# Kernel optimization log

Measured on AMD Instinct MI355X. Metric: run time of the kernel, lower is better.

Reference implementation:

```python
import jax, jax.numpy as jnp
import numpy as np

N0, N1, N2 = 331776, 36864, 4096   # src nodes block0, mid nodes, final items
E0, E1, EP = 294912, 32768, 4096   # edges block0, block1, pos/neg edges
F_RAW, D, H = 128, 256, 512        # raw feat dim, hidden_dims_sum, 2*hidden
N_NODES = 1000000                  # global graph node count (scorer bias)


def setup_inputs() -> dict:
    key = jax.random.key(0)
    ks = jax.random.split(key, 24)
    ri = lambda k, n, hi: jax.random.randint(k, (n,), 0, hi, dtype=jnp.int64 if False else jnp.int32).astype(jnp.int32)
    s = 0.05
    return {
        "feat0": jax.random.normal(ks[0], (N0, F_RAW), jnp.float32),
        "feat_dst": jax.random.normal(ks[1], (N2, F_RAW), jnp.float32),
        "weights0": jax.random.uniform(ks[2], (E0,), jnp.float32),
        "weights1": jax.random.uniform(ks[3], (E1,), jnp.float32),
        "W_proj": jax.random.normal(ks[4], (F_RAW, D), jnp.float32) * s,
        "b_proj": jnp.zeros((D,), jnp.float32),
        "Q1": jax.random.normal(ks[5], (D, H), jnp.float32) * s,
        "bq1": jnp.zeros((H,), jnp.float32),
        "W1": jax.random.normal(ks[6], (D + H, D), jnp.float32) * s,
        "bw1": jnp.zeros((D,), jnp.float32),
        "Q2": jax.random.normal(ks[7], (D, H), jnp.float32) * s,
        "bq2": jnp.zeros((H,), jnp.float32),
        "W2": jax.random.normal(ks[8], (D + H, D), jnp.float32) * s,
        "bw2": jnp.zeros((D,), jnp.float32),
        "bias": jnp.zeros((N_NODES,), jnp.float32),
        "block0_src": ri(ks[9], E0, N0),
        "block0_dst": ri(ks[10], E0, N1),
        "block1_src": ri(ks[11], E1, N1),
        "block1_dst": ri(ks[12], E1, N2),
        "pos_src": ri(ks[13], EP, N2),
        "pos_dst": ri(ks[14], EP, N2),
        "neg_src": ri(ks[15], EP, N2),
        "neg_dst": ri(ks[16], EP, N2),
        "nid": ri(ks[17], N2, N_NODES),
    }


def _l2norm(z):
    n = jnp.linalg.norm(z, axis=1, keepdims=True)
    return z / jnp.where(n == 0, 1.0, n)


def _sage_conv(h_src, h_dst, src, dst, w, Q, bq, W, bw, n_dst):
    # WeightedSAGEConv (dropout omitted: eval-mode deterministic reference)
    n = jax.nn.relu(h_src @ Q + bq)                                   # [N_src, H]
    m = jax.ops.segment_sum(n[src] * w[:, None], dst, num_segments=n_dst)
    ws = jnp.clip(jax.ops.segment_sum(w, dst, num_segments=n_dst), 1.0, None)
    z = jax.nn.relu(jnp.concatenate([m / ws[:, None], h_dst], axis=1) @ W + bw)
    return _l2norm(z)


def _score(h, src, dst, nid, bias):
    # ItemToItemScorer: u_dot_v + src/dst node bias
    return jnp.sum(h[src] * h[dst], axis=1) + bias[nid[src]] + bias[nid[dst]]


def reference(feat0, feat_dst, weights0, weights1, W_proj, b_proj, Q1, bq1, W1, bw1,
              Q2, bq2, W2, bw2, bias, block0_src, block0_dst, block1_src, block1_dst,
              pos_src, pos_dst, neg_src, neg_dst, nid):
    h = feat0 @ W_proj + b_proj                                         # LinearProjector
    h = _sage_conv(h, h[:N1], block0_src, block0_dst, weights0, Q1, bq1, W1, bw1, N1)
    h = _sage_conv(h, h[:N2], block1_src, block1_dst, weights1, Q2, bq2, W2, bw2, N2)
    h_item = (feat_dst @ W_proj + b_proj) + h                           # get_repr skip-add
    pos_score = _score(h_item, pos_src, pos_dst, nid, bias)
    neg_score = _score(h_item, neg_src, neg_dst, nid, bias)
    return (pos_score, neg_score)
```

## Files before the change

kernel.cpp:

```cpp
#include <hip/hip_runtime.h>
#include <hip/hip_bf16.h>

typedef __hip_bfloat16 bf16;
typedef __attribute__((ext_vector_type(8))) short frag8;
typedef __attribute__((ext_vector_type(4))) float f32x4;

#define N0c 331776
#define N1c 36864
#define N2c 4096
#define E0c 294912
#define E1c 32768

__device__ __forceinline__ float bfbits2f(unsigned short b) {
    union { unsigned u; float f; } x; x.u = ((unsigned)b) << 16; return x.f;
}
__device__ __forceinline__ unsigned short f2bfbits(float f) {
    bf16 h = __float2bfloat16(f);
    return *reinterpret_cast<unsigned short*>(&h);
}
__device__ __forceinline__ void load4f(const float* p, float* o) {
    const float4 v = *reinterpret_cast<const float4*>(p);
    o[0] = v.x; o[1] = v.y; o[2] = v.z; o[3] = v.w;
}
__device__ __forceinline__ ushort4 pack4(float4 v) {
    ushort4 o; o.x = f2bfbits(v.x); o.y = f2bfbits(v.y);
    o.z = f2bfbits(v.z); o.w = f2bfbits(v.w); return o;
}
__device__ __forceinline__ void store_c(float* p, float v) { *p = v; }
__device__ __forceinline__ void store_c(bf16* p, float v)  { *p = __float2bfloat16(v); }
__device__ __forceinline__ f32x4 zero4() {
    f32x4 z; z[0] = 0.f; z[1] = 0.f; z[2] = 0.f; z[3] = 0.f; return z;
}
__device__ __forceinline__ f32x4 mfma16(frag8 a, frag8 b, f32x4 c) {
    return __builtin_amdgcn_mfma_f32_16x16x32_bf16(a, b, c, 0, 0, 0);
}

__global__ __launch_bounds__(256) void transpose_bf16(
    const float* __restrict__ src, bf16* __restrict__ dst, int K, int N)
{
    const int idx = blockIdx.x * 256 + threadIdx.x;
    if (idx >= K * N) return;
    const int k = idx / N, n = idx - k * N;
    dst[(size_t)n * K + k] = __float2bfloat16(src[idx]);
}

__global__ __launch_bounds__(256) void hist_kernel(
    const int* __restrict__ dst, int* __restrict__ cnt, int E)
{
    const int e = blockIdx.x * 256 + threadIdx.x;
    if (e < E) atomicAdd(&cnt[dst[e]], 1);
}

__global__ __launch_bounds__(256) void scan_kernel(
    const int* __restrict__ cnt, int* __restrict__ base, int n)
{
    __shared__ int ps[256];
    const int t = threadIdx.x;
    const int chunk = (n + 255) >> 8;
    const int lo = t * chunk;
    const int hi = (lo + chunk < n) ? lo + chunk : n;
    int s = 0;
    for (int i = lo; i < hi; ++i) s += cnt[i];
    ps[t] = s;
    __syncthreads();
    for (int off = 1; off < 256; off <<= 1) {
        int v = (t >= off) ? ps[t - off] : 0;
        __syncthreads();
        ps[t] += v;
        __syncthreads();
    }
    int run = ps[t] - s;
    for (int i = lo; i < hi; ++i) { base[i] = run; run += cnt[i]; }
    if (t == 255) base[n] = ps[255];
}

__global__ __launch_bounds__(256) void fill_kernel(
    const int* __restrict__ dst, const int* __restrict__ base,
    int* __restrict__ cursor, int* __restrict__ perm, int E)
{
    const int e = blockIdx.x * 256 + threadIdx.x;
    if (e < E) {
        const int d = dst[e];
        const int p = base[d] + atomicAdd(&cursor[d], 1);
        perm[p] = e;
    }
}

template<typename TC>
__global__ __launch_bounds__(256) void gemm_mfma_proj(
    const float* __restrict__ A, const bf16* __restrict__ WpT,
    const float* __restrict__ bp, TC* __restrict__ C)
{
    __shared__ bf16 Xs[64 * 136];
    __shared__ bf16 Cs[64 * 264];

    const int tid = threadIdx.x;
    const int lane = tid & 63, wave = tid >> 6;
    const int row0 = blockIdx.x * 64;

    {
        const int r = tid >> 2, q = tid & 3;
        const float* ar = A + (size_t)(row0 + r) * 128 + q * 32;
        bf16* xr = Xs + r * 136 + q * 32;
        #pragma unroll
        for (int i = 0; i < 8; ++i)
            *reinterpret_cast<ushort4*>(xr + i * 4) =
                pack4(*reinterpret_cast<const float4*>(ar + i * 4));
    }
    __syncthreads();

    const int lr = lane & 15;
    const int lk = (lane >> 4) * 8;
    const int lm4 = (lane >> 4) * 4;

    f32x4 acc[4][4];
    #pragma unroll
    for (int mi = 0; mi < 4; ++mi)
        #pragma unroll
        for (int ni = 0; ni < 4; ++ni) acc[mi][ni] = zero4();

    #pragma unroll
    for (int kk = 0; kk < 4; ++kk) {
        frag8 a[4], b[4];
        #pragma unroll
        for (int mi = 0; mi < 4; ++mi)
            a[mi] = *reinterpret_cast<const frag8*>(&Xs[(mi * 16 + lr) * 136 + kk * 32 + lk]);
        #pragma unroll
        for (int ni = 0; ni < 4; ++ni)
            b[ni] = *reinterpret_cast<const frag8*>(
                WpT + (size_t)(wave * 64 + ni * 16 + lr) * 128 + kk * 32 + lk);
        #pragma unroll
        for (int mi = 0; mi < 4; ++mi)
            #pragma unroll
            for (int ni = 0; ni < 4; ++ni)
                acc[mi][ni] = mfma16(a[mi], b[ni], acc[mi][ni]);
    }

    if constexpr (sizeof(TC) == 2) {
        #pragma unroll
        for (int ni = 0; ni < 4; ++ni) {
            const int c = wave * 64 + ni * 16 + lr;
            const float bb = bp[c];
            #pragma unroll
            for (int mi = 0; mi < 4; ++mi)
                #pragma unroll
                for (int i = 0; i < 4; ++i)
                    Cs[(mi * 16 + lm4 + i) * 264 + c] =
                        __float2bfloat16(acc[mi][ni][i] + bb);
        }
        __syncthreads();
        const int r = tid >> 2, q = tid & 3;
        const bf16* sl = Cs + r * 264 + q * 64;
        bf16* dg = (bf16*)C + (size_t)(row0 + r) * 256 + q * 64;
        #pragma unroll
        for (int i = 0; i < 8; ++i)
            *reinterpret_cast<int4*>(dg + i * 8) =
                *reinterpret_cast<const int4*>(sl + i * 8);
    } else {
        #pragma unroll
        for (int ni = 0; ni < 4; ++ni) {
            const int c = wave * 64 + ni * 16 + lr;
            const float bb = bp[c];
            #pragma unroll
            for (int mi = 0; mi < 4; ++mi)
                #pragma unroll
                for (int i = 0; i < 4; ++i)
                    store_c(C + (size_t)(row0 + mi * 16 + lm4 + i) * 256 + c,
                            acc[mi][ni][i] + bb);
        }
    }
}

__global__ __launch_bounds__(256) void edge_csr(
    const bf16* __restrict__ zn, const bf16* __restrict__ QT,
    const float* __restrict__ bq,
    const int* __restrict__ perm, const int* __restrict__ src,
    const float* __restrict__ w,
    bf16* __restrict__ nbuf)
{
    __shared__ bf16 Zs[64 * 264];
    __shared__ bf16 Os[64 * 264];
    __shared__ int   srcs[64];
    __shared__ float wts[64];

    const int tid = threadIdx.x;
    const int lane = tid & 63, wave = tid >> 6;
    const size_t p0 = (size_t)blockIdx.x * 64;

    if (tid < 64) {
        const int e = perm[p0 + tid];
        srcs[tid] = src[e];
        wts[tid]  = w[e];
    }
    __syncthreads();

    {
        const int r = tid >> 2, q = tid & 3;
        const bf16* zr = zn + (size_t)srcs[r] * 256 + q * 64;
        bf16* zo = Zs + r * 264 + q * 64;
        #pragma unroll
        for (int i = 0; i < 16; ++i)
            *reinterpret_cast<ushort4*>(zo + i * 4) =
                *reinterpret_cast<const ushort4*>(zr + i * 4);
    }
    __syncthreads();

    const int lr = lane & 15;
    const int lk = (lane >> 4) * 8;
    const int lm4 = (lane >> 4) * 4;

    for (int pass = 0; pass < 2; ++pass) {
        const int nc0 = wave * 128 + pass * 64;
        f32x4 acc[4][4];
        #pragma unroll
        for (int mi = 0; mi < 4; ++mi)
            #pragma unroll
            for (int ni = 0; ni < 4; ++ni) acc[mi][ni] = zero4();

        #pragma unroll
        for (int kk = 0; kk < 8; ++kk) {
            frag8 a[4], b[4];
            #pragma unroll
            for (int mi = 0; mi < 4; ++mi)
                a[mi] = *reinterpret_cast<const frag8*>(&Zs[(mi * 16 + lr) * 264 + kk * 32 + lk]);
            #pragma unroll
            for (int ni = 0; ni < 4; ++ni)
                b[ni] = *reinterpret_cast<const frag8*>(
                    QT + (size_t)(nc0 + ni * 16 + lr) * 256 + kk * 32 + lk);
            #pragma unroll
            for (int mi = 0; mi < 4; ++mi)
                #pragma unroll
                for (int ni = 0; ni < 4; ++ni)
                    acc[mi][ni] = mfma16(a[mi], b[ni], acc[mi][ni]);
        }

        #pragma unroll
        for (int ni = 0; ni < 4; ++ni) {
            const int gc = nc0 + ni * 16 + lr;
            const float bb = bq[gc];
            const int lc = wave * 64 + ni * 16 + lr;
            #pragma unroll
            for (int mi = 0; mi < 4; ++mi)
                #pragma unroll
                for (int i = 0; i < 4; ++i) {
                    const int row = mi * 16 + lm4 + i;
                    const float val = fmaxf(acc[mi][ni][i] + bb, 0.f) * wts[row];
                    Os[row * 264 + lc] = __float2bfloat16(val);
                }
        }
        __syncthreads();

        {
            const int r = tid >> 2, q = tid & 3;
            const bf16* so = Os + r * 264 + q * 64;
            bf16* dg = nbuf + (p0 + r) * 512 + q * 128 + pass * 64;
            #pragma unroll
            for (int i = 0; i < 8; ++i)
                *reinterpret_cast<int4*>(dg + i * 8) =
                    *reinterpret_cast<const int4*>(so + i * 8);
        }
        __syncthreads();
    }
}

__global__ __launch_bounds__(256) void reduce_csr(
    const bf16* __restrict__ nbuf, const int* __restrict__ base,
    const int* __restrict__ perm, const float* __restrict__ w,
    bf16* __restrict__ mout)
{
    const int d = blockIdx.x;
    const int lo = base[d], hi = base[d + 1];
    __shared__ float s_inv;
    if (threadIdx.x == 0) {
        float s = 0.f;
        for (int k = lo; k < hi; ++k) s += w[perm[k]];
        s_inv = 1.f / fmaxf(s, 1.f);
    }
    __syncthreads();
    const int c = threadIdx.x * 2;
    float a0 = 0.f, a1 = 0.f;
    for (int k = lo; k < hi; ++k) {
        const ushort2 u = *reinterpret_cast<const ushort2*>(nbuf + (size_t)k * 512 + c);
        a0 += bfbits2f(u.x); a1 += bfbits2f(u.y);
    }
    ushort2 o; o.x = f2bfbits(a0 * s_inv); o.y = f2bfbits(a1 * s_inv);
    *reinterpret_cast<ushort2*>(mout + (size_t)d * 512 + c) = o;
}

template<typename TC>
__global__ __launch_bounds__(256) void gemm_mfma_concat(
    const bf16* __restrict__ m, const bf16* __restrict__ hdst,
    const bf16* __restrict__ WT, const float* __restrict__ bias,
    TC* __restrict__ C)
{
    __shared__ bf16 As[64 * 136];

    const int tid = threadIdx.x;
    const int lane = tid & 63, wave = tid >> 6;
    const int row0 = blockIdx.x * 64;
    const int r = tid >> 2, q = tid & 3;

    const int lr = lane & 15;
    const int lk = (lane >> 4) * 8;
    const int lm4 = (lane >> 4) * 4;

    f32x4 acc[4][4];
    #pragma unroll
    for (int mi = 0; mi < 4; ++mi)
        #pragma unroll
        for (int ni = 0; ni < 4; ++ni) acc[mi][ni] = zero4();

    #pragma unroll
    for (int ch = 0; ch < 6; ++ch) {
        bf16* xr = As + r * 136 + q * 32;
        const bf16* srcp = (ch < 4)
            ? m    + (size_t)(row0 + r) * 512 + ch * 128 + q * 32
            : hdst + (size_t)(row0 + r) * 256 + (ch - 4) * 128 + q * 32;
        #pragma unroll
        for (int i = 0; i < 8; ++i)
            *reinterpret_cast<ushort4*>(xr + i * 4) =
                *reinterpret_cast<const ushort4*>(srcp + i * 4);
        __syncthreads();

        #pragma unroll
        for (int kk = 0; kk < 4; ++kk) {
            frag8 a[4], b[4];
            #pragma unroll
            for (int mi = 0; mi < 4; ++mi)
                a[mi] = *reinterpret_cast<const frag8*>(&As[(mi * 16 + lr) * 136 + kk * 32 + lk]);
            #pragma unroll
            for (int ni = 0; ni < 4; ++ni)
                b[ni] = *reinterpret_cast<const frag8*>(
                    WT + (size_t)(wave * 64 + ni * 16 + lr) * 768 + ch * 128 + kk * 32 + lk);
            #pragma unroll
            for (int mi = 0; mi < 4; ++mi)
                #pragma unroll
                for (int ni = 0; ni < 4; ++ni)
                    acc[mi][ni] = mfma16(a[mi], b[ni], acc[mi][ni]);
        }
        __syncthreads();
    }

    #pragma unroll
    for (int ni = 0; ni < 4; ++ni) {
        const int c = wave * 64 + ni * 16 + lr;
        const float bb = bias[c];
        #pragma unroll
        for (int mi = 0; mi < 4; ++mi)
            #pragma unroll
            for (int i = 0; i < 4; ++i)
                store_c(C + (size_t)(row0 + mi * 16 + lm4 + i) * 256 + c,
                        fmaxf(acc[mi][ni][i] + bb, 0.f));
    }
}

__global__ __launch_bounds__(256) void l2norm_kernel(
    const bf16* __restrict__ Z, bf16* __restrict__ out, int rows)
{
    const int wave = threadIdx.x >> 6, lane = threadIdx.x & 63;
    const int row = blockIdx.x * 4 + wave;
    if (row >= rows) return;
    const ushort4 u = *reinterpret_cast<const ushort4*>(Z + (size_t)row * 256 + lane * 4);
    float v[4] = { bfbits2f(u.x), bfbits2f(u.y), bfbits2f(u.z), bfbits2f(u.w) };
    float ss = v[0]*v[0] + v[1]*v[1] + v[2]*v[2] + v[3]*v[3];
    #pragma unroll
    for (int off = 32; off; off >>= 1) ss += __shfl_xor(ss, off, 64);
    const float scale = (ss == 0.f) ? 1.f : (1.f / sqrtf(ss));
    ushort4 o;
    o.x = f2bfbits(v[0]*scale); o.y = f2bfbits(v[1]*scale);
    o.z = f2bfbits(v[2]*scale); o.w = f2bfbits(v[3]*scale);
    *reinterpret_cast<ushort4*>(out + (size_t)row * 256 + lane * 4) = o;
}

__global__ __launch_bounds__(256) void l2norm_add_kernel(
    const float* __restrict__ Z, const float* __restrict__ P,
    float* __restrict__ out, int rows)
{
    const int wave = threadIdx.x >> 6, lane = threadIdx.x & 63;
    const int row = blockIdx.x * 4 + wave;
    if (row >= rows) return;
    float v[4];
    load4f(Z + (size_t)row * 256 + lane * 4, v);
    float ss = v[0]*v[0] + v[1]*v[1] + v[2]*v[2] + v[3]*v[3];
    #pragma unroll
    for (int off = 32; off; off >>= 1) ss += __shfl_xor(ss, off, 64);
    const float scale = (ss == 0.f) ? 1.f : (1.f / sqrtf(ss));
    float p[4];
    load4f(P + (size_t)row * 256 + lane * 4, p);
    float4 o;
    o.x = p[0] + v[0]*scale; o.y = p[1] + v[1]*scale;
    o.z = p[2] + v[2]*scale; o.w = p[3] + v[3]*scale;
    *reinterpret_cast<float4*>(out + (size_t)row * 256 + lane * 4) = o;
}

__global__ __launch_bounds__(256) void score_kernel(
    const float* __restrict__ h,
    const int* __restrict__ ps, const int* __restrict__ pdi,
    const int* __restrict__ ns, const int* __restrict__ nd,
    const int* __restrict__ nid, const float* __restrict__ bias,
    float* __restrict__ out)
{
    const int wave = threadIdx.x >> 6, lane = threadIdx.x & 63;
    const int e = blockIdx.x * 4 + wave;
    const int ei = e & 4095;
    const int s = (e < 4096) ? ps[ei] : ns[ei];
    const int d = (e < 4096) ? pdi[ei] : nd[ei];
    float a[4], b[4];
    load4f(h + (size_t)s * 256 + lane * 4, a);
    load4f(h + (size_t)d * 256 + lane * 4, b);
    float dot = a[0]*b[0] + a[1]*b[1] + a[2]*b[2] + a[3]*b[3];
    #pragma unroll
    for (int off = 32; off; off >>= 1) dot += __shfl_xor(dot, off, 64);
    if (lane == 0)
        out[e] = dot + bias[nid[s]] + bias[nid[d]];
}

extern "C" void kernel_launch(void* const* d_in, const int* in_sizes, int n_in,
                              void* d_out, int out_size, void* d_ws, size_t ws_size,
                              hipStream_t stream)
{
    const float* feat0    = (const float*)d_in[0];
    const float* feat_dst = (const float*)d_in[1];
    const float* weights0 = (const float*)d_in[2];
    const float* weights1 = (const float*)d_in[3];
    const float* W_proj   = (const float*)d_in[4];
    const float* b_proj   = (const float*)d_in[5];
    const float* Q1       = (const float*)d_in[6];
    const float* bq1      = (const float*)d_in[7];
    const float* W1       = (const float*)d_in[8];
    const float* bw1      = (const float*)d_in[9];
    const float* Q2       = (const float*)d_in[10];
    const float* bq2      = (const float*)d_in[11];
    const float* W2       = (const float*)d_in[12];
    const float* bw2      = (const float*)d_in[13];
    const float* biasN    = (const float*)d_in[14];
    const int* b0s = (const int*)d_in[15];
    const int* b0d = (const int*)d_in[16];
    const int* b1s = (const int*)d_in[17];
    const int* b1d = (const int*)d_in[18];
    const int* pos_src = (const int*)d_in[19];
    const int* pos_dst = (const int*)d_in[20];
    const int* neg_src = (const int*)d_in[21];
    const int* neg_dst = (const int*)d_in[22];
    const int* nid     = (const int*)d_in[23];

    char* ws = (char*)d_ws;
    size_t off = 0;
    auto alloc = [&](size_t bytes) -> void* {
        void* p = ws + off; off += (bytes + 255) & ~(size_t)255; return p;
    };
    bf16* h0    = (bf16*)alloc((size_t)N0c * 256 * 2);
    char* r2    = (char*)alloc((size_t)E0c * 512 * 2);
    bf16* m1    = (bf16*)alloc((size_t)N1c * 512 * 2);
    bf16* WpT   = (bf16*)alloc((size_t)256 * 128 * 2);
    bf16* Q1T   = (bf16*)alloc((size_t)512 * 256 * 2);
    bf16* Q2T   = (bf16*)alloc((size_t)512 * 256 * 2);
    bf16* W1T   = (bf16*)alloc((size_t)256 * 768 * 2);
    bf16* W2T   = (bf16*)alloc((size_t)256 * 768 * 2);
    int*  cnt    = (int*)alloc((size_t)(N1c + 1) * 4);
    int*  base   = (int*)alloc((size_t)(N1c + 1) * 4);
    int*  cursor = (int*)alloc((size_t)N1c * 4);
    int*  perm   = (int*)alloc((size_t)E0c * 4);

    bf16* nbuf1 = (bf16*)r2;
    bf16* z1b   = (bf16*)r2;
    bf16* z1n   = (bf16*)(r2 + 18874368);
    bf16* nbuf2 = (bf16*)(r2 + 37748736);
    bf16* m2    = (bf16*)(r2 + 71303168);
    float* z2     = (float*)(r2 + 75497472);
    float* pdbuf  = (float*)(r2 + 79691776);
    float* h_item = (float*)(r2 + 83886080);

    transpose_bf16<<<(128*256 + 255)/256, 256, 0, stream>>>(W_proj, WpT, 128, 256);
    transpose_bf16<<<(256*512 + 255)/256, 256, 0, stream>>>(Q1, Q1T, 256, 512);
    transpose_bf16<<<(256*512 + 255)/256, 256, 0, stream>>>(Q2, Q2T, 256, 512);
    transpose_bf16<<<(768*256 + 255)/256, 256, 0, stream>>>(W1, W1T, 768, 256);
    transpose_bf16<<<(768*256 + 255)/256, 256, 0, stream>>>(W2, W2T, 768, 256);

    gemm_mfma_proj<bf16><<<N0c/64, 256, 0, stream>>>(feat0, WpT, b_proj, h0);

    hipMemsetAsync(cnt,    0, (size_t)N1c * 4, stream);
    hipMemsetAsync(cursor, 0, (size_t)N1c * 4, stream);
    hist_kernel<<<E0c/256, 256, 0, stream>>>(b0d, cnt, E0c);
    scan_kernel<<<1, 256, 0, stream>>>(cnt, base, N1c);
    fill_kernel<<<E0c/256, 256, 0, stream>>>(b0d, base, cursor, perm, E0c);

    edge_csr<<<E0c/64, 256, 0, stream>>>(h0, Q1T, bq1, perm, b0s, weights0, nbuf1);

    reduce_csr<<<N1c, 256, 0, stream>>>(nbuf1, base, perm, weights0, m1);

    gemm_mfma_concat<bf16><<<N1c/64, 256, 0, stream>>>(m1, h0, W1T, bw1, z1b);

    l2norm_kernel<<<N1c/4, 256, 0, stream>>>(z1b, z1n, N1c);

    hipMemsetAsync(cnt,    0, (size_t)N2c * 4, stream);
    hipMemsetAsync(cursor, 0, (size_t)N2c * 4, stream);
    hist_kernel<<<E1c/256, 256, 0, stream>>>(b1d, cnt, E1c);
    scan_kernel<<<1, 256, 0, stream>>>(cnt, base, N2c);
    fill_kernel<<<E1c/256, 256, 0, stream>>>(b1d, base, cursor, perm, E1c);

    edge_csr<<<E1c/64, 256, 0, stream>>>(z1n, Q2T, bq2, perm, b1s, weights1, nbuf2);

    reduce_csr<<<N2c, 256, 0, stream>>>(nbuf2, base, perm, weights1, m2);

    gemm_mfma_concat<float><<<N2c/64, 256, 0, stream>>>(m2, z1n, W2T, bw2, z2);

    gemm_mfma_proj<float><<<N2c/64, 256, 0, stream>>>(feat_dst, WpT, b_proj, pdbuf);

    l2norm_add_kernel<<<N2c/4, 256, 0, stream>>>(z2, pdbuf, h_item, N2c);

    score_kernel<<<2048, 256, 0, stream>>>(
        h_item, pos_src, pos_dst, neg_src, neg_dst, nid, biasN, (float*)d_out);
}
```

Before: 834.5 us.

## Fuse input projection into layer-1 edge kernel and trim scans, epilogues, reductions

Drops the full projection of all 331776 source nodes. The layer-1 edge kernel now gathers raw features per edge and projects them in place, and only the first N1 rows are projected for the destination input. It also widens the scan to 1024 threads with int4 loads, writes edge outputs straight to global memory without staging in shared memory, and parallelises the weight-sum in reduce_csr across a wavefront. These changes cut memory traffic and launch-serial work, but each edge now recomputes its projection GEMM, and the direct global stores are less coalesced.

```diff
diff --git a/kernel.cpp b/kernel.cpp
--- a/kernel.cpp
+++ b/kernel.cpp
@@ -51,19 +51,22 @@
     if (e < E) atomicAdd(&cnt[dst[e]], 1);
 }
 
-__global__ __launch_bounds__(256) void scan_kernel(
+__global__ __launch_bounds__(1024) void scan_kernel(
     const int* __restrict__ cnt, int* __restrict__ base, int n)
 {
-    __shared__ int ps[256];
+    __shared__ int ps[1024];
     const int t = threadIdx.x;
-    const int chunk = (n + 255) >> 8;
+    const int chunk = (n + 1023) >> 10;
     const int lo = t * chunk;
     const int hi = (lo + chunk < n) ? lo + chunk : n;
     int s = 0;
-    for (int i = lo; i < hi; ++i) s += cnt[i];
+    for (int i = lo; i < hi; i += 4) {
+        const int4 v = *reinterpret_cast<const int4*>(cnt + i);
+        s += v.x + v.y + v.z + v.w;
+    }
     ps[t] = s;
     __syncthreads();
-    for (int off = 1; off < 256; off <<= 1) {
+    for (int off = 1; off < 1024; off <<= 1) {
         int v = (t >= off) ? ps[t - off] : 0;
         __syncthreads();
         ps[t] += v;
@@ -71,7 +74,7 @@
     }
     int run = ps[t] - s;
     for (int i = lo; i < hi; ++i) { base[i] = run; run += cnt[i]; }
-    if (t == 255) base[n] = ps[255];
+    if (t == 1023) base[n] = ps[1023];
 }
 
 __global__ __launch_bounds__(256) void fill_kernel(
@@ -92,7 +95,6 @@
     const float* __restrict__ bp, TC* __restrict__ C)
 {
     __shared__ bf16 Xs[64 * 136];
-    __shared__ bf16 Cs[64 * 264];
 
     const int tid = threadIdx.x;
     const int lane = tid & 63, wave = tid >> 6;
@@ -136,7 +138,80 @@
                 acc[mi][ni] = mfma16(a[mi], b[ni], acc[mi][ni]);
     }
 
-    if constexpr (sizeof(TC) == 2) {
+    #pragma unroll
+    for (int ni = 0; ni < 4; ++ni) {
+        const int c = wave * 64 + ni * 16 + lr;
+        const float bb = bp[c];
+        #pragma unroll
+        for (int mi = 0; mi < 4; ++mi)
+            #pragma unroll
+            for (int i = 0; i < 4; ++i)
+                store_c(C + (size_t)(row0 + mi * 16 + lm4 + i) * 256 + c,
+                        acc[mi][ni][i] + bb);
+    }
+}
+
+__global__ __launch_bounds__(256) void edge_csr_l1(
+    const float* __restrict__ feat0, const bf16* __restrict__ WpT,
+    const float* __restrict__ bp, const bf16* __restrict__ Q1T,
+    const float* __restrict__ bq,
+    const int* __restrict__ perm, const int* __restrict__ src,
+    const float* __restrict__ w, bf16* __restrict__ nbuf)
+{
+    __shared__ bf16 Xs[64 * 136];
+    __shared__ bf16 Hs[64 * 264];
+    __shared__ int   srcs[64];
+    __shared__ float wts[64];
+
+    const int tid = threadIdx.x;
+    const int lane = tid & 63, wave = tid >> 6;
+    const size_t p0 = (size_t)blockIdx.x * 64;
+
+    if (tid < 64) {
+        const int e = perm[p0 + tid];
+        srcs[tid] = src[e];
+        wts[tid]  = w[e];
+    }
+    __syncthreads();
+
+    {
+        const int r = tid >> 2, q = tid & 3;
+        const float* fr = feat0 + (size_t)srcs[r] * 128 + q * 32;
+        bf16* xr = Xs + r * 136 + q * 32;
+        #pragma unroll
+        for (int i = 0; i < 8; ++i)
+            *reinterpret_cast<ushort4*>(xr + i * 4) =
+                pack4(*reinterpret_cast<const float4*>(fr + i * 4));
+    }
+    __syncthreads();
+
+    const int lr = lane & 15;
+    const int lk = (lane >> 4) * 8;
+    const int lm4 = (lane >> 4) * 4;
+
+    {
+        f32x4 acc[4][4];
+        #pragma unroll
+        for (int mi = 0; mi < 4; ++mi)
+            #pragma unroll
+            for (int ni = 0; ni < 4; ++ni) acc[mi][ni] = zero4();
+
+        #pragma unroll
+        for (int kk = 0; kk < 4; ++kk) {
+            frag8 a[4], b[4];
+            #pragma unroll
+            for (int mi = 0; mi < 4; ++mi)
+                a[mi] = *reinterpret_cast<const frag8*>(&Xs[(mi * 16 + lr) * 136 + kk * 32 + lk]);
+            #pragma unroll
+            for (int ni = 0; ni < 4; ++ni)
+                b[ni] = *reinterpret_cast<const frag8*>(
+                    WpT + (size_t)(wave * 64 + ni * 16 + lr) * 128 + kk * 32 + lk);
+            #pragma unroll
+            for (int mi = 0; mi < 4; ++mi)
+                #pragma unroll
+                for (int ni = 0; ni < 4; ++ni)
+                    acc[mi][ni] = mfma16(a[mi], b[ni], acc[mi][ni]);
+        }
         #pragma unroll
         for (int ni = 0; ni < 4; ++ni) {
             const int c = wave * 64 + ni * 16 + lr;
@@ -145,28 +220,48 @@
             for (int mi = 0; mi < 4; ++mi)
                 #pragma unroll
                 for (int i = 0; i < 4; ++i)
-                    Cs[(mi * 16 + lm4 + i) * 264 + c] =
+                    Hs[(mi * 16 + lm4 + i) * 264 + c] =
                         __float2bfloat16(acc[mi][ni][i] + bb);
         }
-        __syncthreads();
-        const int r = tid >> 2, q = tid & 3;
-        const bf16* sl = Cs + r * 264 + q * 64;
-        bf16* dg = (bf16*)C + (size_t)(row0 + r) * 256 + q * 64;
-        #pragma unroll
-        for (int i = 0; i < 8; ++i)
-            *reinterpret_cast<int4*>(dg + i * 8) =
-                *reinterpret_cast<const int4*>(sl + i * 8);
-    } else {
+    }
+    __syncthreads();
+
+    for (int pass = 0; pass < 2; ++pass) {
+        const int nc0 = wave * 128 + pass * 64;
+        f32x4 acc[4][4];
+        #pragma unroll
+        for (int mi = 0; mi < 4; ++mi)
+            #pragma unroll
+            for (int ni = 0; ni < 4; ++ni) acc[mi][ni] = zero4();
+
+        #pragma unroll
+        for (int kk = 0; kk < 8; ++kk) {
+            frag8 a[4], b[4];
+            #pragma unroll
+            for (int mi = 0; mi < 4; ++mi)
+                a[mi] = *reinterpret_cast<const frag8*>(&Hs[(mi * 16 + lr) * 264 + kk * 32 + lk]);
+            #pragma unroll
+            for (int ni = 0; ni < 4; ++ni)
+                b[ni] = *reinterpret_cast<const frag8*>(
+                    Q1T + (size_t)(nc0 + ni * 16 + lr) * 256 + kk * 32 + lk);
+            #pragma unroll
+            for (int mi = 0; mi < 4; ++mi)
+                #pragma unroll
+                for (int ni = 0; ni < 4; ++ni)
+                    acc[mi][ni] = mfma16(a[mi], b[ni], acc[mi][ni]);
+        }
         #pragma unroll
         for (int ni = 0; ni < 4; ++ni) {
-            const int c = wave * 64 + ni * 16 + lr;
-            const float bb = bp[c];
-            #pragma unroll
-            for (int mi = 0; mi < 4; ++mi)
-                #pragma unroll
-                for (int i = 0; i < 4; ++i)
-                    store_c(C + (size_t)(row0 + mi * 16 + lm4 + i) * 256 + c,
-                            acc[mi][ni][i] + bb);
+            const int gc = nc0 + ni * 16 + lr;
+            const float bb = bq[gc];
+            #pragma unroll
+            for (int mi = 0; mi < 4; ++mi)
+                #pragma unroll
+                for (int i = 0; i < 4; ++i) {
+                    const int row = mi * 16 + lm4 + i;
+                    const float val = fmaxf(acc[mi][ni][i] + bb, 0.f) * wts[row];
+                    nbuf[(p0 + row) * 512 + gc] = __float2bfloat16(val);
+                }
         }
     }
 }
@@ -179,7 +274,6 @@
     bf16* __restrict__ nbuf)
 {
     __shared__ bf16 Zs[64 * 264];
-    __shared__ bf16 Os[64 * 264];
     __shared__ int   srcs[64];
     __shared__ float wts[64];
 
@@ -233,33 +327,19 @@
                 for (int ni = 0; ni < 4; ++ni)
                     acc[mi][ni] = mfma16(a[mi], b[ni], acc[mi][ni]);
         }
-
         #pragma unroll
         for (int ni = 0; ni < 4; ++ni) {
             const int gc = nc0 + ni * 16 + lr;
             const float bb = bq[gc];
-            const int lc = wave * 64 + ni * 16 + lr;
             #pragma unroll
             for (int mi = 0; mi < 4; ++mi)
                 #pragma unroll
                 for (int i = 0; i < 4; ++i) {
                     const int row = mi * 16 + lm4 + i;
                     const float val = fmaxf(acc[mi][ni][i] + bb, 0.f) * wts[row];
-                    Os[row * 264 + lc] = __float2bfloat16(val);
+                    nbuf[(p0 + row) * 512 + gc] = __float2bfloat16(val);
                 }
         }
-        __syncthreads();
-
-        {
-            const int r = tid >> 2, q = tid & 3;
-            const bf16* so = Os + r * 264 + q * 64;
-            bf16* dg = nbuf + (p0 + r) * 512 + q * 128 + pass * 64;
-            #pragma unroll
-            for (int i = 0; i < 8; ++i)
-                *reinterpret_cast<int4*>(dg + i * 8) =
-                    *reinterpret_cast<const int4*>(so + i * 8);
-        }
-        __syncthreads();
     }
 }
 
@@ -271,10 +351,12 @@
     const int d = blockIdx.x;
     const int lo = base[d], hi = base[d + 1];
     __shared__ float s_inv;
-    if (threadIdx.x == 0) {
+    if (threadIdx.x < 64) {
         float s = 0.f;
-        for (int k = lo; k < hi; ++k) s += w[perm[k]];
-        s_inv = 1.f / fmaxf(s, 1.f);
+        for (int k = lo + threadIdx.x; k < hi; k += 64) s += w[perm[k]];
+        #pragma unroll
+        for (int off = 32; off; off >>= 1) s += __shfl_xor(s, off, 64);
+        if (threadIdx.x == 0) s_inv = 1.f / fmaxf(s, 1.f);
     }
     __syncthreads();
     const int c = threadIdx.x * 2;
@@ -449,7 +531,7 @@
     auto alloc = [&](size_t bytes) -> void* {
         void* p = ws + off; off += (bytes + 255) & ~(size_t)255; return p;
     };
-    bf16* h0    = (bf16*)alloc((size_t)N0c * 256 * 2);
+    bf16* h1dst = (bf16*)alloc((size_t)N1c * 256 * 2);
     char* r2    = (char*)alloc((size_t)E0c * 512 * 2);
     bf16* m1    = (bf16*)alloc((size_t)N1c * 512 * 2);
     bf16* WpT   = (bf16*)alloc((size_t)256 * 128 * 2);
@@ -477,26 +559,27 @@
     transpose_bf16<<<(768*256 + 255)/256, 256, 0, stream>>>(W1, W1T, 768, 256);
     transpose_bf16<<<(768*256 + 255)/256, 256, 0, stream>>>(W2, W2T, 768, 256);
 
-    gemm_mfma_proj<bf16><<<N0c/64, 256, 0, stream>>>(feat0, WpT, b_proj, h0);
+    gemm_mfma_proj<bf16><<<N1c/64, 256, 0, stream>>>(feat0, WpT, b_proj, h1dst);
 
     hipMemsetAsync(cnt,    0, (size_t)N1c * 4, stream);
     hipMemsetAsync(cursor, 0, (size_t)N1c * 4, stream);
     hist_kernel<<<E0c/256, 256, 0, stream>>>(b0d, cnt, E0c);
-    scan_kernel<<<1, 256, 0, stream>>>(cnt, base, N1c);
+    scan_kernel<<<1, 1024, 0, stream>>>(cnt, base, N1c);
     fill_kernel<<<E0c/256, 256, 0, stream>>>(b0d, base, cursor, perm, E0c);
 
-    edge_csr<<<E0c/64, 256, 0, stream>>>(h0, Q1T, bq1, perm, b0s, weights0, nbuf1);
+    edge_csr_l1<<<E0c/64, 256, 0, stream>>>(
+        feat0, WpT, b_proj, Q1T, bq1, perm, b0s, weights0, nbuf1);
 
     reduce_csr<<<N1c, 256, 0, stream>>>(nbuf1, base, perm, weights0, m1);
 
-    gemm_mfma_concat<bf16><<<N1c/64, 256, 0, stream>>>(m1, h0, W1T, bw1, z1b);
+    gemm_mfma_concat<bf16><<<N1c/64, 256, 0, stream>>>(m1, h1dst, W1T, bw1, z1b);
 
     l2norm_kernel<<<N1c/4, 256, 0, stream>>>(z1b, z1n, N1c);
 
     hipMemsetAsync(cnt,    0, (size_t)N2c * 4, stream);
     hipMemsetAsync(cursor, 0, (size_t)N2c * 4, stream);
     hist_kernel<<<E1c/256, 256, 0, stream>>>(b1d, cnt, E1c);
-    scan_kernel<<<1, 256, 0, stream>>>(cnt, base, N2c);
+    scan_kernel<<<1, 1024, 0, stream>>>(cnt, base, N2c);
     fill_kernel<<<E1c/256, 256, 0, stream>>>(b1d, base, cursor, perm, E1c);
 
     edge_csr<<<E1c/64, 256, 0, stream>>>(z1n, Q2T, bq2, perm, b1s, weights1, nbuf2);
```

Result: faster. 798.5 us (-4.3%).
